# Kernel optimization log

Measured on AMD Instinct MI355X. Metric: run time of the kernel, lower is better.

The kernel has to match this reference:

```python
import jax, jax.numpy as jnp
import numpy as np

N, M, D = 8192, 8192, 128

def setup_inputs() -> dict:
    key = jax.random.key(0)
    kx, ky = jax.random.split(key)
    x = jax.random.normal(kx, (N, D), dtype=jnp.float32)
    y = jax.random.normal(ky, (M, D), dtype=jnp.float32)
    return {"x": x, "y": y}

def reference(x, y):
    # Pairwise squared L2 distance: same math as expand-sub-square-sum,
    # computed via the x^2 + y^2 - 2xy rewrite (GEMM for the cross term).
    x_sq = jnp.sum(x * x, axis=1)              # [n]
    y_sq = jnp.sum(y * y, axis=1)              # [m]
    cross = jnp.einsum('nd,md->nm', x, y)      # [n, m]
    dist = x_sq[:, None] + y_sq[None, :] - 2.0 * cross
    return dist
```

## Files before the change

### kernel.cpp

```cpp
#include <hip/hip_runtime.h>
#include <hip/hip_bf16.h>


typedef __attribute__((ext_vector_type(8))) short short8;
typedef __attribute__((ext_vector_type(4))) float f32x4;

#define NROW 8192
#define DIM  128

__device__ __forceinline__ short f2bf(float f) {
    unsigned u = __builtin_bit_cast(unsigned, f);
    unsigned r = u + 0x7FFFu + ((u >> 16) & 1u);
    return (short)(r >> 16);
}

__device__ __forceinline__ void barrier_lgkm() {
    asm volatile("s_waitcnt lgkmcnt(0)" ::: "memory");
    __builtin_amdgcn_s_barrier();
    __builtin_amdgcn_sched_barrier(0);
}

__global__ __launch_bounds__(256)
void prep_kernel(const float* __restrict__ X, const float* __restrict__ Y,
                 unsigned short* __restrict__ Xp, unsigned short* __restrict__ Yp,
                 float* __restrict__ xn, float* __restrict__ yn)
{
    const int t   = blockIdx.x * 256 + threadIdx.x;
    const int sel = t >> 17;
    const int c   = t & 131071;
    const int row = c >> 4;
    const int sub = c & 15;

    const float* src = (sel ? Y : X) + (size_t)row * DIM + sub * 8;
    f32x4 v0 = ((const f32x4*)src)[0];
    f32x4 v1 = ((const f32x4*)src)[1];

    short8 p;
    p[0]=f2bf(v0[0]); p[1]=f2bf(v0[1]); p[2]=f2bf(v0[2]); p[3]=f2bf(v0[3]);
    p[4]=f2bf(v1[0]); p[5]=f2bf(v1[1]); p[6]=f2bf(v1[2]); p[7]=f2bf(v1[3]);

    float part = v0[0]*v0[0] + v0[1]*v0[1] + v0[2]*v0[2] + v0[3]*v0[3]
               + v1[0]*v1[0] + v1[1]*v1[1] + v1[2]*v1[2] + v1[3]*v1[3];
    part += __shfl_xor(part, 1, 16);
    part += __shfl_xor(part, 2, 16);
    part += __shfl_xor(part, 4, 16);
    part += __shfl_xor(part, 8, 16);

    const int g = row >> 4, lr = row & 15, kk = sub >> 2, lg = sub & 3;
    unsigned short* dst = (sel ? Yp : Xp) + (size_t)(((g*4 + kk)*64) + lg*16 + lr) * 8;
    *(short8*)dst = p;
    if (sub == 0) (sel ? yn : xn)[row] = part;
}

__global__ __launch_bounds__(256, 3)
void dist_main(const unsigned short* __restrict__ Xp,
               const unsigned short* __restrict__ Yp,
               const float* __restrict__ xn, const float* __restrict__ yn,
               float* __restrict__ out)
{
    __shared__ char lds[16 * 2048];

    const int bid = blockIdx.x;
    const int wg  = (bid & 7) * 512 + (bid >> 3);
    const int R0  = (wg >> 4) * 32;
    const int C0  = (wg & 15) * 512;

    const int t    = threadIdx.x;
    const int w    = t >> 6, lane = t & 63;
    const int lr   = lane & 15, lg = lane >> 4;

    const short8* Ap = (const short8*)Xp;
    const short8* Bp = (const short8*)Yp;
    const int ga = R0 >> 4;
    const int gb = (C0 >> 4) + w * 8;

    f32x4 acc[2][8];
    #pragma unroll
    for (int j = 0; j < 2; ++j)
        #pragma unroll
        for (int i = 0; i < 8; ++i)
            acc[j][i] = (f32x4){0.f, 0.f, 0.f, 0.f};

    #pragma unroll
    for (int kk = 0; kk < 4; ++kk) {
        short8 a0 = Ap[(size_t)(ga * 4 + kk) * 64 + lane];
        short8 a1 = Ap[(size_t)((ga + 1) * 4 + kk) * 64 + lane];
        #pragma unroll
        for (int half = 0; half < 2; ++half) {
            short8 b[4];
            #pragma unroll
            for (int i = 0; i < 4; ++i)
                b[i] = Bp[(size_t)((gb + half * 4 + i) * 4 + kk) * 64 + lane];
            #pragma unroll
            for (int i = 0; i < 4; ++i) {
                acc[0][half * 4 + i] = __builtin_amdgcn_mfma_f32_16x16x32_bf16(b[i], a0, acc[0][half * 4 + i], 0, 0, 0);
                acc[1][half * 4 + i] = __builtin_amdgcn_mfma_f32_16x16x32_bf16(b[i], a1, acc[1][half * 4 + i], 0, 0, 0);
            }
        }
    }

    float xnv[2];
    xnv[0] = xn[R0 + lr];
    xnv[1] = xn[R0 + 16 + lr];
    f32x4 ynv[8];
    #pragma unroll
    for (int i = 0; i < 8; ++i)
        ynv[i] = *(const f32x4*)(yn + C0 + w * 128 + i * 16 + lg * 4);

    #pragma unroll
    for (int p = 0; p < 2; ++p) {
        #pragma unroll
        for (int i = 0; i < 8; ++i) {
            f32x4 o;
            #pragma unroll
            for (int r = 0; r < 4; ++r)
                o[r] = xnv[p] + ynv[i][r] - 2.0f * acc[p][i][r];
            const int slotb = w * 512 + i * 64 + lg * 16;
            *(f32x4*)(lds + lr * 2048 + (slotb ^ ((lr & 7) << 4))) = o;
        }
        barrier_lgkm();
        #pragma unroll
        for (int rr = 0; rr < 4; ++rr) {
            const int lrow = w * 4 + rr;
            const size_t gbase = (size_t)(R0 + p * 16 + lrow) * NROW + C0;
            #pragma unroll
            for (int h = 0; h < 2; ++h) {
                const int s16 = h * 64 + lane;
                f32x4 v = *(const f32x4*)(lds + lrow * 2048 + ((s16 * 16) ^ ((lrow & 7) << 4)));
                __builtin_nontemporal_store(v, (f32x4*)(out + gbase + s16 * 4));
            }
        }
        if (p == 0) barrier_lgkm();
    }
}

__global__ __launch_bounds__(256, 2)
void dist_fallback(const float* __restrict__ X, const float* __restrict__ Y,
                   float* __restrict__ out)
{
    __shared__ unsigned short As[128 * DIM];
    __shared__ unsigned short Bs[128 * DIM];
    __shared__ float xs[128];
    __shared__ float ys[128];

    const int t = threadIdx.x, bid = blockIdx.x;
    const int R0 = (bid >> 6) * 128, C0 = (bid & 63) * 128;
    {
        const float* gx = X + (size_t)R0 * DIM;
        const float* gy = Y + (size_t)C0 * DIM;
        char* lx = (char*)As; char* ly = (char*)Bs;
        #pragma unroll
        for (int i = 0; i < 8; ++i) {
            int q = i * 256 + t, r = q >> 4, c = q & 15;
            f32x4 a0 = ((const f32x4*)(gx + q*8))[0], a1 = ((const f32x4*)(gx + q*8))[1];
            f32x4 b0 = ((const f32x4*)(gy + q*8))[0], b1 = ((const f32x4*)(gy + q*8))[1];
            short8 pa, pb;
            #pragma unroll
            for (int e = 0; e < 4; ++e) { pa[e]=f2bf(a0[e]); pa[e+4]=f2bf(a1[e]); pb[e]=f2bf(b0[e]); pb[e+4]=f2bf(b1[e]); }
            int off = r * 256 + ((c * 16) ^ ((r & 7) << 4));
            *(short8*)(lx + off) = pa; *(short8*)(ly + off) = pb;
        }
    }
    {
        const float* row = (t < 128) ? (X + (size_t)(R0 + t) * DIM) : (Y + (size_t)(C0 + t - 128) * DIM);
        float s = 0.f;
        #pragma unroll
        for (int i = 0; i < DIM; i += 4) { f32x4 v = *(const f32x4*)(row + i); s += v[0]*v[0]+v[1]*v[1]+v[2]*v[2]+v[3]*v[3]; }
        if (t < 128) xs[t] = s; else ys[t - 128] = s;
    }
    __syncthreads();
    const int wid = t >> 6, lane = t & 63, wr = wid >> 1, wc = wid & 1, lg = lane >> 4, lrr = lane & 15;
    f32x4 acc[4][4];
    #pragma unroll
    for (int i = 0; i < 4; ++i) for (int j = 0; j < 4; ++j) acc[i][j] = (f32x4){0,0,0,0};
    const char* lA = (const char*)As; const char* lB = (const char*)Bs;
    #pragma unroll
    for (int kk = 0; kk < 4; ++kk) {
        const int kb = kk * 64 + lg * 16;
        short8 a[4], b[4];
        #pragma unroll
        for (int i = 0; i < 4; ++i) {
            int ar = wr*64 + i*16 + lrr; a[i] = *(const short8*)(lA + ar*256 + (kb ^ ((ar&7)<<4)));
            int br = wc*64 + i*16 + lrr; b[i] = *(const short8*)(lB + br*256 + (kb ^ ((br&7)<<4)));
        }
        #pragma unroll
        for (int i = 0; i < 4; ++i) for (int j = 0; j < 4; ++j)
            acc[i][j] = __builtin_amdgcn_mfma_f32_16x16x32_bf16(a[i], b[j], acc[i][j], 0, 0, 0);
    }
    #pragma unroll
    for (int i = 0; i < 4; ++i) for (int j = 0; j < 4; ++j) {
        const int row_l = wr*64 + i*16 + lg*4, col_l = wc*64 + j*16 + lrr;
        const float yv = ys[col_l];
        float* po = out + (size_t)(R0 + row_l) * NROW + (C0 + col_l);
        #pragma unroll
        for (int r = 0; r < 4; ++r) po[(size_t)r * NROW] = xs[row_l + r] + yv - 2.0f * acc[i][j][r];
    }
}

extern "C" void kernel_launch(void* const* d_in, const int* in_sizes, int n_in,
                              void* d_out, int out_size, void* d_ws, size_t ws_size,
                              hipStream_t stream) {
    const float* x = (const float*)d_in[0];
    const float* y = (const float*)d_in[1];
    float* out = (float*)d_out;

    const size_t XP_OFF = 0;
    const size_t YP_OFF = 2097152;
    const size_t XN_OFF = 4194304;
    const size_t YN_OFF = 4194304 + 32768;
    const size_t NEED   = 4194304 + 65536;

    if (ws_size >= NEED) {
        char* w = (char*)d_ws;
        unsigned short* Xp = (unsigned short*)(w + XP_OFF);
        unsigned short* Yp = (unsigned short*)(w + YP_OFF);
        float* xnp = (float*)(w + XN_OFF);
        float* ynp = (float*)(w + YN_OFF);
        prep_kernel<<<1024, 256, 0, stream>>>(x, y, Xp, Yp, xnp, ynp);
        dist_main<<<4096, 256, 0, stream>>>(Xp, Yp, xnp, ynp, out);
    } else {
        dist_fallback<<<4096, 256, 0, stream>>>(x, y, out);
    }
}
```

Measured before the change: 59.04 us.

## Reshape dist_main tile to 16x1024 with single A fragment per wave

Changes each workgroup's output tile from 32 rows x 512 columns to 16 rows x 1024 columns. Each wave now loads one A fragment and sixteen B fragments per k-step instead of two A and eight B. The LDS staging for the epilogue is reorganised into two passes of 8 rows x 4096 bytes, and only half the lanes write in each pass. This lengthens contiguous row stores and changes the A/B reuse balance, but it raises B-operand global loads per output and leaves lanes idle during the LDS writes.

```diff
diff --git a/kernel.cpp b/kernel.cpp
--- a/kernel.cpp
+++ b/kernel.cpp
@@ -58,12 +58,12 @@
                const float* __restrict__ xn, const float* __restrict__ yn,
                float* __restrict__ out)
 {
-    __shared__ char lds[16 * 2048];
+    __shared__ char lds[8 * 4096];
 
     const int bid = blockIdx.x;
     const int wg  = (bid & 7) * 512 + (bid >> 3);
-    const int R0  = (wg >> 4) * 32;
-    const int C0  = (wg & 15) * 512;
+    const int R0  = (wg >> 3) * 16;
+    const int C0  = (wg & 7) * 1024;
 
     const int t    = threadIdx.x;
     const int w    = t >> 6, lane = t & 63;
@@ -72,62 +72,55 @@
     const short8* Ap = (const short8*)Xp;
     const short8* Bp = (const short8*)Yp;
     const int ga = R0 >> 4;
-    const int gb = (C0 >> 4) + w * 8;
-
-    f32x4 acc[2][8];
-    #pragma unroll
-    for (int j = 0; j < 2; ++j)
-        #pragma unroll
-        for (int i = 0; i < 8; ++i)
-            acc[j][i] = (f32x4){0.f, 0.f, 0.f, 0.f};
+    const int gb = (C0 >> 4) + w * 16;
+
+    f32x4 acc[16];
+    #pragma unroll
+    for (int i = 0; i < 16; ++i)
+        acc[i] = (f32x4){0.f, 0.f, 0.f, 0.f};
 
     #pragma unroll
     for (int kk = 0; kk < 4; ++kk) {
-        short8 a0 = Ap[(size_t)(ga * 4 + kk) * 64 + lane];
-        short8 a1 = Ap[(size_t)((ga + 1) * 4 + kk) * 64 + lane];
-        #pragma unroll
-        for (int half = 0; half < 2; ++half) {
+        short8 a = Ap[(size_t)(ga * 4 + kk) * 64 + lane];
+        #pragma unroll
+        for (int q = 0; q < 4; ++q) {
             short8 b[4];
             #pragma unroll
             for (int i = 0; i < 4; ++i)
-                b[i] = Bp[(size_t)((gb + half * 4 + i) * 4 + kk) * 64 + lane];
-            #pragma unroll
-            for (int i = 0; i < 4; ++i) {
-                acc[0][half * 4 + i] = __builtin_amdgcn_mfma_f32_16x16x32_bf16(b[i], a0, acc[0][half * 4 + i], 0, 0, 0);
-                acc[1][half * 4 + i] = __builtin_amdgcn_mfma_f32_16x16x32_bf16(b[i], a1, acc[1][half * 4 + i], 0, 0, 0);
+                b[i] = Bp[(size_t)((gb + q * 4 + i) * 4 + kk) * 64 + lane];
+            #pragma unroll
+            for (int i = 0; i < 4; ++i)
+                acc[q * 4 + i] = __builtin_amdgcn_mfma_f32_16x16x32_bf16(b[i], a, acc[q * 4 + i], 0, 0, 0);
+        }
+    }
+
+    const float xv = xn[R0 + lr];
+
+    #pragma unroll
+    for (int p = 0; p < 2; ++p) {
+        if ((lr >> 3) == p) {
+            const int rl = lr & 7;
+            #pragma unroll
+            for (int i = 0; i < 16; ++i) {
+                f32x4 yv = *(const f32x4*)(yn + C0 + w * 256 + i * 16 + lg * 4);
+                f32x4 o;
+                #pragma unroll
+                for (int r = 0; r < 4; ++r)
+                    o[r] = xv + yv[r] - 2.0f * acc[i][r];
+                const int slotb = (w * 64 + i * 4 + lg) * 16;
+                *(f32x4*)(lds + rl * 4096 + (slotb ^ (rl << 4))) = o;
             }
         }
-    }
-
-    float xnv[2];
-    xnv[0] = xn[R0 + lr];
-    xnv[1] = xn[R0 + 16 + lr];
-    f32x4 ynv[8];
-    #pragma unroll
-    for (int i = 0; i < 8; ++i)
-        ynv[i] = *(const f32x4*)(yn + C0 + w * 128 + i * 16 + lg * 4);
-
-    #pragma unroll
-    for (int p = 0; p < 2; ++p) {
-        #pragma unroll
-        for (int i = 0; i < 8; ++i) {
-            f32x4 o;
-            #pragma unroll
-            for (int r = 0; r < 4; ++r)
-                o[r] = xnv[p] + ynv[i][r] - 2.0f * acc[p][i][r];
-            const int slotb = w * 512 + i * 64 + lg * 16;
-            *(f32x4*)(lds + lr * 2048 + (slotb ^ ((lr & 7) << 4))) = o;
-        }
         barrier_lgkm();
         #pragma unroll
-        for (int rr = 0; rr < 4; ++rr) {
-            const int lrow = w * 4 + rr;
-            const size_t gbase = (size_t)(R0 + p * 16 + lrow) * NROW + C0;
-            #pragma unroll
-            for (int h = 0; h < 2; ++h) {
-                const int s16 = h * 64 + lane;
-                f32x4 v = *(const f32x4*)(lds + lrow * 2048 + ((s16 * 16) ^ ((lrow & 7) << 4)));
-                __builtin_nontemporal_store(v, (f32x4*)(out + gbase + s16 * 4));
+        for (int rr = 0; rr < 2; ++rr) {
+            const int rl = w * 2 + rr;
+            const size_t gbase = (size_t)(R0 + p * 8 + rl) * NROW + C0;
+            #pragma unroll
+            for (int h = 0; h < 4; ++h) {
+                const int chunk = h * 64 + lane;
+                f32x4 v = *(const f32x4*)(lds + rl * 4096 + ((chunk * 16) ^ (rl << 4)));
+                __builtin_nontemporal_store(v, (f32x4*)(out + gbase + chunk * 4));
             }
         }
         if (p == 0) barrier_lgkm();
```

Result: slower. 96.69 us (+63.8%).

## Make dist kernel persistent and overlap previous tile stores with next tile MFMA

Applied to the files above, without the earlier changes.

Launches 512 workgroups instead of 4096, and each one loops over 8 row bands of 32 rows sharing one 512-column slice. The epilogue goes into a doubled 64KB LDS buffer, and the previous band's global stores are interleaved into the next band's MFMA k-loop, with a drain at the end. The aim is to hide output-store latency behind compute and to reuse the y-norm loads across bands. In exchange, occupancy drops to 2 blocks per CU, there are fewer blocks to balance load, and barriers are added each iteration.

```diff
diff --git a/kernel.cpp b/kernel.cpp
--- a/kernel.cpp
+++ b/kernel.cpp
@@ -52,85 +52,108 @@
     if (sub == 0) (sel ? yn : xn)[row] = part;
 }
 
-__global__ __launch_bounds__(256, 3)
+__global__ __launch_bounds__(256, 2)
 void dist_main(const unsigned short* __restrict__ Xp,
                const unsigned short* __restrict__ Yp,
                const float* __restrict__ xn, const float* __restrict__ yn,
                float* __restrict__ out)
 {
-    __shared__ char lds[16 * 2048];
+    __shared__ char lds[32 * 2048];
 
     const int bid = blockIdx.x;
-    const int wg  = (bid & 7) * 512 + (bid >> 3);
-    const int R0  = (wg >> 4) * 32;
-    const int C0  = (wg & 15) * 512;
-
-    const int t    = threadIdx.x;
-    const int w    = t >> 6, lane = t & 63;
-    const int lr   = lane & 15, lg = lane >> 4;
+    const int xcd = bid & 7;
+    const int s   = bid >> 3;
+    const int t   = threadIdx.x;
+    const int w   = t >> 6, lane = t & 63;
+    const int lr  = lane & 15, lg = lane >> 4;
 
     const short8* Ap = (const short8*)Xp;
     const short8* Bp = (const short8*)Yp;
-    const int ga = R0 >> 4;
-    const int gb = (C0 >> 4) + w * 8;
-
-    f32x4 acc[2][8];
-    #pragma unroll
-    for (int j = 0; j < 2; ++j)
-        #pragma unroll
-        for (int i = 0; i < 8; ++i)
-            acc[j][i] = (f32x4){0.f, 0.f, 0.f, 0.f};
-
-    #pragma unroll
-    for (int kk = 0; kk < 4; ++kk) {
-        short8 a0 = Ap[(size_t)(ga * 4 + kk) * 64 + lane];
-        short8 a1 = Ap[(size_t)((ga + 1) * 4 + kk) * 64 + lane];
-        #pragma unroll
-        for (int half = 0; half < 2; ++half) {
-            short8 b[4];
-            #pragma unroll
-            for (int i = 0; i < 4; ++i)
-                b[i] = Bp[(size_t)((gb + half * 4 + i) * 4 + kk) * 64 + lane];
-            #pragma unroll
-            for (int i = 0; i < 4; ++i) {
-                acc[0][half * 4 + i] = __builtin_amdgcn_mfma_f32_16x16x32_bf16(b[i], a0, acc[0][half * 4 + i], 0, 0, 0);
-                acc[1][half * 4 + i] = __builtin_amdgcn_mfma_f32_16x16x32_bf16(b[i], a1, acc[1][half * 4 + i], 0, 0, 0);
-            }
-        }
-    }
-
-    float xnv[2];
-    xnv[0] = xn[R0 + lr];
-    xnv[1] = xn[R0 + 16 + lr];
+
+    const int C0    = (s & 15) * 512;
+    const int gb    = (C0 >> 4) + w * 8;
+    const int band0 = xcd * 32 + (s >> 4);
+
     f32x4 ynv[8];
     #pragma unroll
     for (int i = 0; i < 8; ++i)
         ynv[i] = *(const f32x4*)(yn + C0 + w * 128 + i * 16 + lg * 4);
 
-    #pragma unroll
-    for (int p = 0; p < 2; ++p) {
-        #pragma unroll
-        for (int i = 0; i < 8; ++i) {
-            f32x4 o;
-            #pragma unroll
-            for (int r = 0; r < 4; ++r)
-                o[r] = xnv[p] + ynv[i][r] - 2.0f * acc[p][i][r];
-            const int slotb = w * 512 + i * 64 + lg * 16;
-            *(f32x4*)(lds + lr * 2048 + (slotb ^ ((lr & 7) << 4))) = o;
-        }
+    int prevR0 = 0;
+
+    for (int st = 0; st < 8; ++st) {
+        const int R0 = (band0 + st * 4) * 32;
+        const int ga = R0 >> 4;
+        const bool do_store = (st > 0);
+
+        f32x4 acc[2][8];
+        #pragma unroll
+        for (int j = 0; j < 2; ++j)
+            #pragma unroll
+            for (int i = 0; i < 8; ++i)
+                acc[j][i] = (f32x4){0.f, 0.f, 0.f, 0.f};
+
+        #pragma unroll
+        for (int kk = 0; kk < 4; ++kk) {
+            short8 a0 = Ap[(size_t)(ga * 4 + kk) * 64 + lane];
+            short8 a1 = Ap[(size_t)((ga + 1) * 4 + kk) * 64 + lane];
+            #pragma unroll
+            for (int half = 0; half < 2; ++half) {
+                short8 b[4];
+                #pragma unroll
+                for (int i = 0; i < 4; ++i)
+                    b[i] = Bp[(size_t)((gb + half * 4 + i) * 4 + kk) * 64 + lane];
+                #pragma unroll
+                for (int i = 0; i < 4; ++i) {
+                    acc[0][half*4+i] = __builtin_amdgcn_mfma_f32_16x16x32_bf16(b[i], a0, acc[0][half*4+i], 0, 0, 0);
+                    acc[1][half*4+i] = __builtin_amdgcn_mfma_f32_16x16x32_bf16(b[i], a1, acc[1][half*4+i], 0, 0, 0);
+                }
+            }
+            if (do_store) {
+                #pragma unroll
+                for (int u = 0; u < 4; ++u) {
+                    const int sid   = kk * 4 + u;
+                    const int rr    = sid >> 1;
+                    const int h     = sid & 1;
+                    const int lrow  = w * 8 + rr;
+                    const int chunk = h * 64 + lane;
+                    f32x4 v = *(const f32x4*)(lds + lrow * 2048 + ((chunk * 16) ^ ((lrow & 7) << 4)));
+                    __builtin_nontemporal_store(v, (f32x4*)(out + (size_t)(prevR0 + lrow) * NROW + C0 + chunk * 4));
+                }
+            }
+            __builtin_amdgcn_sched_barrier(0);
+        }
+
         barrier_lgkm();
-        #pragma unroll
-        for (int rr = 0; rr < 4; ++rr) {
-            const int lrow = w * 4 + rr;
-            const size_t gbase = (size_t)(R0 + p * 16 + lrow) * NROW + C0;
-            #pragma unroll
-            for (int h = 0; h < 2; ++h) {
-                const int s16 = h * 64 + lane;
-                f32x4 v = *(const f32x4*)(lds + lrow * 2048 + ((s16 * 16) ^ ((lrow & 7) << 4)));
-                __builtin_nontemporal_store(v, (f32x4*)(out + gbase + s16 * 4));
+
+        const float xv0 = xn[R0 + lr];
+        const float xv1 = xn[R0 + 16 + lr];
+        #pragma unroll
+        for (int p = 0; p < 2; ++p) {
+            const int row = p * 16 + lr;
+            const float xv = p ? xv1 : xv0;
+            #pragma unroll
+            for (int i = 0; i < 8; ++i) {
+                f32x4 o;
+                #pragma unroll
+                for (int r = 0; r < 4; ++r)
+                    o[r] = xv + ynv[i][r] - 2.0f * acc[p][i][r];
+                const int slotb = w * 512 + i * 64 + lg * 16;
+                *(f32x4*)(lds + row * 2048 + (slotb ^ ((row & 7) << 4))) = o;
             }
         }
-        if (p == 0) barrier_lgkm();
+        barrier_lgkm();
+        prevR0 = R0;
+    }
+
+    #pragma unroll
+    for (int sid = 0; sid < 16; ++sid) {
+        const int rr    = sid >> 1;
+        const int h     = sid & 1;
+        const int lrow  = w * 8 + rr;
+        const int chunk = h * 64 + lane;
+        f32x4 v = *(const f32x4*)(lds + lrow * 2048 + ((chunk * 16) ^ ((lrow & 7) << 4)));
+        __builtin_nontemporal_store(v, (f32x4*)(out + (size_t)(prevR0 + lrow) * NROW + C0 + chunk * 4));
     }
 }
 
@@ -217,7 +240,7 @@
         float* xnp = (float*)(w + XN_OFF);
         float* ynp = (float*)(w + YN_OFF);
         prep_kernel<<<1024, 256, 0, stream>>>(x, y, Xp, Yp, xnp, ynp);
-        dist_main<<<4096, 256, 0, stream>>>(Xp, Yp, xnp, ynp, out);
+        dist_main<<<512, 256, 0, stream>>>(Xp, Yp, xnp, ynp, out);
     } else {
         dist_fallback<<<4096, 256, 0, stream>>>(x, y, out);
     }
```

Measured after the change: 69.02 us, median of 3. 16.9% more time.
